# Kernel optimization log

Measured on AMD Instinct MI355X. Metric: run time of the kernel, lower is better.

Reference implementation:

```python
import math
import jax, jax.numpy as jnp
import numpy as np


def _skew(X, pad_value):
    # shift every row i one step right relative to row i-1: [B,M,L] -> [B,M,M+L]
    B, M, L = X.shape
    X = jnp.pad(X, ((0, 0), (0, 0), (0, M + 1)), constant_values=pad_value)
    X = X.reshape(B, -1)[:, :-M]
    return X.reshape(B, M, M + L)


def _unskew(X):
    # reverse of _skew: [B,M,M+L] -> [B,M,L]
    B, M, ML = X.shape
    L = ML - M
    X = X.reshape(B, -1)
    X = jnp.pad(X, ((0, 0), (0, M)))
    X = X.reshape(B, M, M + L + 1)
    return X[:, :, :L]


def setup_inputs() -> dict:
    key0 = jax.random.key(0)
    k1, k2, k3, k4 = jax.random.split(key0, 4)
    BH, M, D = 64, 1024, 64          # batch*heads, block len, head dim
    L = 1024                          # attn_span
    return {
        "query": jax.random.normal(k1, (BH, M, D), dtype=jnp.float32),
        "key": jax.random.normal(k2, (BH, M + L, D), dtype=jnp.float32),
        "value": jax.random.normal(k3, (BH, M + L, D), dtype=jnp.float32),
        "key_pe": jax.random.normal(k4, (1, D, L), dtype=jnp.float32),
    }


def reference(query, key, value, key_pe):
    hidden_size = query.shape[-1]
    # content scores: [BH, M, M+L] -> banded [BH, M, L]
    attn_cont = _unskew(jnp.matmul(query, jnp.swapaxes(key, -1, -2)))
    # relative position scores: [BH, M, L] (key_pe broadcasts over batch)
    attn_pos = jnp.matmul(query, key_pe)
    attn = (attn_cont + attn_pos) / math.sqrt(hidden_size)
    attn = jax.nn.softmax(attn, axis=-1)
    # dropout p=0.0 -> identity
    attn_skew = _skew(attn, 0.0)          # [BH, M, M+L]
    out = jnp.matmul(attn_skew, value)    # [BH, M, D]
    return out
```

## Files before the change

kernel.cpp:

```cpp
#include <hip/hip_runtime.h>
#include <hip/hip_bf16.h>


typedef __attribute__((ext_vector_type(8))) short bf16x8;
typedef __attribute__((ext_vector_type(4))) short bf16x4;
typedef __attribute__((ext_vector_type(4))) float f32x4;

#define BHN   64
#define MQ    1024
#define DH    64
#define LS    1024
#define NKEY  2048
#define NTILE 17

#define SZ_PE  ((size_t)LS * DH * 2)
#define OFF_K  SZ_PE
#define SZ_K   ((size_t)BHN * NKEY * DH * 2)
#define OFF_V  (OFF_K + SZ_K)
#define SZ_V   ((size_t)BHN * DH * NKEY * 2)
#define WS_NEED (OFF_V + SZ_V)

#define SCL_LOG2E 0.18033688011112042f

__device__ __forceinline__ short f2bf(float f) {
  unsigned u = __float_as_uint(f);
  u += 0x7FFFu + ((u >> 16) & 1u);
  return (short)(u >> 16);
}
__device__ __forceinline__ void async_copy16(const void* g, void* l) {
  __builtin_amdgcn_global_load_lds((const __attribute__((address_space(1))) void*)g,
                                   (__attribute__((address_space(3))) void*)l, 16, 0, 0);
}

__global__ void prep_pe_kernel(const float* __restrict__ pe, short* __restrict__ peT) {
  const int idx = blockIdx.x * 256 + threadIdx.x;
  const int rel = idx >> 6, d = idx & 63;
  peT[rel * 64 + (((d >> 3) ^ (rel & 7)) * 8) + (d & 7)] = f2bf(pe[d * LS + rel]);
}

__global__ void prep_k_kernel(const float* __restrict__ K, short* __restrict__ Kb) {
  const size_t i = ((size_t)blockIdx.x * 256 + threadIdx.x) * 4;
  const int row = (int)(i >> 6);
  const int col = (int)(i & 63);
  float4 f = *(const float4*)(K + i);
  bf16x4 b = {f2bf(f.x), f2bf(f.y), f2bf(f.z), f2bf(f.w)};
  *(bf16x4*)(Kb + (size_t)row * 64 + (((col >> 3) ^ (row & 7)) * 8) + (col & 7)) = b;
}

__global__ __launch_bounds__(256) void prep_v_kernel(const float* __restrict__ V,
                                                     short* __restrict__ Vb) {
  __shared__ short st[64 * 68];
  const int bh = blockIdx.y, jt = blockIdx.x;
  const int r = threadIdx.x >> 2, cb = (threadIdx.x & 3) * 16;
  const float* src = V + ((size_t)bh * NKEY + jt * 64 + r) * DH + cb;
#pragma unroll
  for (int c = 0; c < 16; c += 4) {
    float4 f = *(const float4*)(src + c);
    bf16x4 b = {f2bf(f.x), f2bf(f.y), f2bf(f.z), f2bf(f.w)};
    *(bf16x4*)&st[r * 68 + cb + c] = b;
  }
  __syncthreads();
  const int d = threadIdx.x >> 2, kb = (threadIdx.x & 3) * 16;
  __attribute__((aligned(16))) short tmp[16];
#pragma unroll
  for (int j = 0; j < 16; ++j) tmp[j] = st[(kb + j) * 68 + d];
  short* dst = Vb + ((size_t)bh * DH + d) * NKEY + jt * 64 + kb;
  *(bf16x8*)dst = *(bf16x8*)&tmp[0];
  *(bf16x8*)(dst + 8) = *(bf16x8*)&tmp[8];
}

template <bool PRECONV>
__global__ __launch_bounds__(256, 4)
void seq_attn_kernel(const float* __restrict__ Qf, const float* __restrict__ Kf,
                     const float* __restrict__ Vf, const short* __restrict__ peT,
                     const short* __restrict__ Kb, const short* __restrict__ Vb,
                     float* __restrict__ Out) {
  __shared__ short sK[64 * 64];
  __shared__ short sPE[2 * 64 * 64];
  __shared__ short sV[64 * 64];
  __shared__ short sPA[64 * 64];

  const int tid  = threadIdx.x;
  const int w    = tid >> 6;
  const int lane = tid & 63;
  const int li   = lane & 15;
  const int quad = lane >> 4;
  const int linear = blockIdx.y * 16 + blockIdx.x;
  const int slot   = linear >> 3;
  const int bh     = (linear & 7) * 8 + (slot >> 4);
  const int i0     = (slot & 15) * 64;
  const int rbase  = w * 16 + quad * 4;

  bf16x8 aq[2];
  {
    const float* qp = Qf + (size_t)((bh * MQ + i0 + w * 16 + li) * DH) + quad * 8;
#pragma unroll
    for (int ks = 0; ks < 2; ++ks) {
      const float4 f0 = *(const float4*)(qp + ks * 32);
      const float4 f1 = *(const float4*)(qp + ks * 32 + 4);
      bf16x8 a;
      a[0] = f2bf(f0.x); a[1] = f2bf(f0.y); a[2] = f2bf(f0.z); a[3] = f2bf(f0.w);
      a[4] = f2bf(f1.x); a[5] = f2bf(f1.y); a[6] = f2bf(f1.z); a[7] = f2bf(f1.w);
      aq[ks] = a;
    }
  }

  float l_i[4] = {0.f, 0.f, 0.f, 0.f};
  f32x4 acco[4];
#pragma unroll
  for (int nt = 0; nt < 4; ++nt) acco[nt] = (f32x4){0.f, 0.f, 0.f, 0.f};

  f32x4 curPw[4];
  f32x4 prevw3;
  prevw3 = (f32x4){0.f, 0.f, 0.f, 0.f};

  for (int t = 0; t < NTILE; ++t) {
    const int j0 = i0 + t * 64;
    __syncthreads();

    if constexpr (PRECONV) {
      {
        const char* gb = (const char*)(Kb + ((size_t)bh * NKEY + j0) * 64);
#pragma unroll
        for (int it = 0; it < 2; ++it) {
          const int c0 = w * 128 + it * 64;
          async_copy16(gb + (size_t)(c0 + lane) * 16, (char*)sK + (size_t)c0 * 16);
        }
      }
      if (t < NTILE - 1) {
        const char* gb = (const char*)(peT + (size_t)t * 64 * 64);
        char* db = (char*)sPE + (size_t)(t & 1) * 8192;
#pragma unroll
        for (int it = 0; it < 2; ++it) {
          const int c0 = w * 128 + it * 64;
          async_copy16(gb + (size_t)(c0 + lane) * 16, db + (size_t)c0 * 16);
        }
      }
      {
#pragma unroll
        for (int it = 0; it < 2; ++it) {
          const int s = w * 128 + it * 64 + lane;
          const int d = s >> 3;
          const int g = (s & 7) ^ (d & 7);
          const short* gp = Vb + ((size_t)bh * DH + d) * NKEY + j0 + g * 8;
          async_copy16(gp, (char*)sV + (size_t)(w * 128 + it * 64) * 16);
        }
      }
    } else {
      {
        const int srow = tid >> 2, l0 = tid & 3, sdb = l0 * 16;
        const float* src = Kf + (size_t)(bh * NKEY + j0 + srow) * DH + sdb;
        const float4 a0 = *(const float4*)(src + 0);
        const float4 a1 = *(const float4*)(src + 4);
        const float4 a2 = *(const float4*)(src + 8);
        const float4 a3 = *(const float4*)(src + 12);
        bf16x8 b0, b1;
        b0[0]=f2bf(a0.x); b0[1]=f2bf(a0.y); b0[2]=f2bf(a0.z); b0[3]=f2bf(a0.w);
        b0[4]=f2bf(a1.x); b0[5]=f2bf(a1.y); b0[6]=f2bf(a1.z); b0[7]=f2bf(a1.w);
        b1[0]=f2bf(a2.x); b1[1]=f2bf(a2.y); b1[2]=f2bf(a2.z); b1[3]=f2bf(a2.w);
        b1[4]=f2bf(a3.x); b1[5]=f2bf(a3.y); b1[6]=f2bf(a3.z); b1[7]=f2bf(a3.w);
        const int s7 = srow & 7;
        *(bf16x8*)&sK[srow * 64 + (((2 * l0)     ^ s7) * 8)] = b0;
        *(bf16x8*)&sK[srow * 64 + (((2 * l0 + 1) ^ s7) * 8)] = b1;
      }
      {
        const int vdb = (tid & 15) * 4, vkb = (tid >> 4) * 4;
        const float* src = Vf + (size_t)(bh * NKEY + j0 + vkb) * DH + vdb;
        const float4 r0 = *(const float4*)(src);
        const float4 r1 = *(const float4*)(src + DH);
        const float4 r2 = *(const float4*)(src + 2 * DH);
        const float4 r3 = *(const float4*)(src + 3 * DH);
        bf16x4 cc[4];
        cc[0] = (bf16x4){ f2bf(r0.x), f2bf(r1.x), f2bf(r2.x), f2bf(r3.x) };
        cc[1] = (bf16x4){ f2bf(r0.y), f2bf(r1.y), f2bf(r2.y), f2bf(r3.y) };
        cc[2] = (bf16x4){ f2bf(r0.z), f2bf(r1.z), f2bf(r2.z), f2bf(r3.z) };
        cc[3] = (bf16x4){ f2bf(r0.w), f2bf(r1.w), f2bf(r2.w), f2bf(r3.w) };
        const int g = vkb >> 3, h = (vkb >> 2) & 1;
#pragma unroll
        for (int jj = 0; jj < 4; ++jj) {
          const int d = vdb + jj;
          *(bf16x4*)&sV[d * 64 + ((g ^ (d & 7)) * 8) + h * 4] = cc[jj];
        }
      }
      if (t < NTILE - 1) {
        const short* src = peT + (size_t)t * 64 * 64;
        short* db = sPE + (size_t)(t & 1) * 4096;
        *(bf16x8*)&db[tid * 16]     = *(const bf16x8*)(src + tid * 16);
        *(bf16x8*)&db[tid * 16 + 8] = *(const bf16x8*)(src + tid * 16 + 8);
      }
    }
    __syncthreads();

#pragma unroll
    for (int m = 0; m < 4; ++m) {
      const int colIdx = 4 * t - w + m;
      const int base = ((colIdx >> 2) & 1) * 4096 + ((colIdx & 3) * 16 + li) * 64;
      f32x4 c = (f32x4){0.f, 0.f, 0.f, 0.f};
#pragma unroll
      for (int ks = 0; ks < 2; ++ks) {
        const int gs = (((ks * 4 + quad) ^ (li & 7)) * 8);
        const bf16x8 b = *(bf16x8*)&sPE[base + gs];
        c = __builtin_amdgcn_mfma_f32_16x16x32_bf16(aq[ks], b, c, 0, 0, 0);
      }
      curPw[m] = c;
    }

    f32x4 cs[4];
#pragma unroll
    for (int nt = 0; nt < 4; ++nt) {
      f32x4 c = (f32x4){0.f, 0.f, 0.f, 0.f};
#pragma unroll
      for (int ks = 0; ks < 2; ++ks) {
        const int gs = (((ks * 4 + quad) ^ (li & 7)) * 8);
        const bf16x8 b = *(bf16x8*)&sK[(nt * 16 + li) * 64 + gs];
        c = __builtin_amdgcn_mfma_f32_16x16x32_bf16(aq[ks], b, c, 0, 0, 0);
      }
      cs[nt] = c;
    }

#pragma unroll
    for (int r = 0; r < 4; ++r) {
      const int e       = li - quad * 4 - r;
      const bool ge     = (e >= 0);
      const int srcLane = quad * 16 + (e & 15);
      const float shm = __shfl(prevw3[r],    srcLane);
      const float sh0 = __shfl(curPw[0][r], srcLane);
      const float sh1 = __shfl(curPw[1][r], srcLane);
      const float sh2 = __shfl(curPw[2][r], srcLane);
      const float sh3 = __shfl(curPw[3][r], srcLane);
      const float pos0 = ge ? sh0 : shm;
      const float pos1 = ge ? sh1 : sh0;
      const float pos2 = ge ? sh2 : sh1;
      const float pos3 = ge ? sh3 : sh2;
      float p0 = __builtin_exp2f((cs[0][r] + pos0) * SCL_LOG2E);
      float p1 = __builtin_exp2f((cs[1][r] + pos1) * SCL_LOG2E);
      float p2 = __builtin_exp2f((cs[2][r] + pos2) * SCL_LOG2E);
      float p3 = __builtin_exp2f((cs[3][r] + pos3) * SCL_LOG2E);
      if (t == 0) {
        p0 = (0 > w || (0 == w && ge)) ? p0 : 0.f;
        p1 = (1 > w || (1 == w && ge)) ? p1 : 0.f;
        p2 = (2 > w || (2 == w && ge)) ? p2 : 0.f;
        p3 = (3 > w || (3 == w && ge)) ? p3 : 0.f;
      } else if (t == NTILE - 1) {
        p0 = (0 < w || (0 == w && !ge)) ? p0 : 0.f;
        p1 = (1 < w || (1 == w && !ge)) ? p1 : 0.f;
        p2 = (2 < w || (2 == w && !ge)) ? p2 : 0.f;
        p3 = (3 < w || (3 == w && !ge)) ? p3 : 0.f;
      }
      l_i[r] += (p0 + p1) + (p2 + p3);
      const int rowA = rbase + r;
      const int sw = (rowA >> 1) & 7;
      sPA[rowA * 64 + (((0 + (li >> 3)) ^ sw) * 8) + (li & 7)] = f2bf(p0);
      sPA[rowA * 64 + (((2 + (li >> 3)) ^ sw) * 8) + (li & 7)] = f2bf(p1);
      sPA[rowA * 64 + (((4 + (li >> 3)) ^ sw) * 8) + (li & 7)] = f2bf(p2);
      sPA[rowA * 64 + (((6 + (li >> 3)) ^ sw) * 8) + (li & 7)] = f2bf(p3);
    }
    prevw3 = curPw[3];

#pragma unroll
    for (int ks = 0; ks < 2; ++ks) {
      const int rowA = w * 16 + li;
      const bf16x8 ap =
          *(bf16x8*)&sPA[rowA * 64 + (((ks * 4 + quad) ^ ((rowA >> 1) & 7)) * 8)];
#pragma unroll
      for (int nt = 0; nt < 4; ++nt) {
        const int d  = nt * 16 + li;
        const int gs = (((ks * 4 + quad) ^ (d & 7)) * 8);
        const bf16x8 bv = *(bf16x8*)&sV[d * 64 + gs];
        acco[nt] = __builtin_amdgcn_mfma_f32_16x16x32_bf16(ap, bv, acco[nt], 0, 0, 0);
      }
    }
  }

#pragma unroll
  for (int r = 0; r < 4; ++r) {
    float l = l_i[r];
    l += __shfl_xor(l, 1);
    l += __shfl_xor(l, 2);
    l += __shfl_xor(l, 4);
    l += __shfl_xor(l, 8);
    const float inv = 1.0f / l;
#pragma unroll
    for (int nt = 0; nt < 4; ++nt) {
      Out[(size_t)(bh * MQ + i0 + rbase + r) * DH + nt * 16 + li] = acco[nt][r] * inv;
    }
  }
}

extern "C" void kernel_launch(void* const* d_in, const int* in_sizes, int n_in,
                              void* d_out, int out_size, void* d_ws, size_t ws_size,
                              hipStream_t stream) {
  const float* q  = (const float*)d_in[0];
  const float* k  = (const float*)d_in[1];
  const float* v  = (const float*)d_in[2];
  const float* pe = (const float*)d_in[3];
  float* out = (float*)d_out;
  short* peT = (short*)d_ws;
  short* Kb  = (short*)((char*)d_ws + OFF_K);
  short* Vb  = (short*)((char*)d_ws + OFF_V);
  const bool preconv = ws_size >= WS_NEED;

  prep_pe_kernel<<<256, 256, 0, stream>>>(pe, peT);
  dim3 grid(MQ / 64, BHN);
  if (preconv) {
    prep_k_kernel<<<8192, 256, 0, stream>>>(k, Kb);
    prep_v_kernel<<<dim3(32, 64), 256, 0, stream>>>(v, Vb);
    seq_attn_kernel<true><<<grid, 256, 0, stream>>>(q, k, v, peT, Kb, Vb, out);
  } else {
    seq_attn_kernel<false><<<grid, 256, 0, stream>>>(q, k, v, peT, Kb, Vb, out);
  }
}
```

Measured before the change: 182.5 us.

## Fuse prep kernels, permute P/V key order for vectorized LDS stores, bf16-pack shuffles

Merges the three preprocessing kernels (PE transpose, K convert, V transpose) into one launch that dispatches on block index, and gives the K conversion 16 elements per thread. The key ordering inside each 64-wide tile is permuted consistently in the V layout and in the P tile, so each lane writes its four probabilities with one 8-byte LDS store instead of four scalar stores. The four position-score shuffles are packed into two by sending pairs of bf16 values, which cuts cross-lane traffic but rounds those position scores to bf16 before they are added.

```diff
diff --git a/kernel.cpp b/kernel.cpp
--- a/kernel.cpp
+++ b/kernel.cpp
@@ -27,46 +27,72 @@
   u += 0x7FFFu + ((u >> 16) & 1u);
   return (short)(u >> 16);
 }
+__device__ __forceinline__ float bf2f(short s) {
+  return __uint_as_float(((unsigned)(unsigned short)s) << 16);
+}
+__device__ __forceinline__ unsigned packbf(float a, float b) {
+  return (unsigned)(unsigned short)f2bf(a) | ((unsigned)(unsigned short)f2bf(b) << 16);
+}
 __device__ __forceinline__ void async_copy16(const void* g, void* l) {
   __builtin_amdgcn_global_load_lds((const __attribute__((address_space(1))) void*)g,
                                    (__attribute__((address_space(3))) void*)l, 16, 0, 0);
 }
 
-__global__ void prep_pe_kernel(const float* __restrict__ pe, short* __restrict__ peT) {
-  const int idx = blockIdx.x * 256 + threadIdx.x;
-  const int rel = idx >> 6, d = idx & 63;
-  peT[rel * 64 + (((d >> 3) ^ (rel & 7)) * 8) + (d & 7)] = f2bf(pe[d * LS + rel]);
-}
-
-__global__ void prep_k_kernel(const float* __restrict__ K, short* __restrict__ Kb) {
-  const size_t i = ((size_t)blockIdx.x * 256 + threadIdx.x) * 4;
-  const int row = (int)(i >> 6);
-  const int col = (int)(i & 63);
-  float4 f = *(const float4*)(K + i);
-  bf16x4 b = {f2bf(f.x), f2bf(f.y), f2bf(f.z), f2bf(f.w)};
-  *(bf16x4*)(Kb + (size_t)row * 64 + (((col >> 3) ^ (row & 7)) * 8) + (col & 7)) = b;
-}
-
-__global__ __launch_bounds__(256) void prep_v_kernel(const float* __restrict__ V,
-                                                     short* __restrict__ Vb) {
+__global__ __launch_bounds__(256)
+void prep_fused(const float* __restrict__ pe, const float* __restrict__ K,
+                const float* __restrict__ V, short* __restrict__ peT,
+                short* __restrict__ Kb, short* __restrict__ Vb) {
   __shared__ short st[64 * 68];
-  const int bh = blockIdx.y, jt = blockIdx.x;
-  const int r = threadIdx.x >> 2, cb = (threadIdx.x & 3) * 16;
-  const float* src = V + ((size_t)bh * NKEY + jt * 64 + r) * DH + cb;
-#pragma unroll
-  for (int c = 0; c < 16; c += 4) {
-    float4 f = *(const float4*)(src + c);
-    bf16x4 b = {f2bf(f.x), f2bf(f.y), f2bf(f.z), f2bf(f.w)};
-    *(bf16x4*)&st[r * 68 + cb + c] = b;
-  }
-  __syncthreads();
-  const int d = threadIdx.x >> 2, kb = (threadIdx.x & 3) * 16;
-  __attribute__((aligned(16))) short tmp[16];
-#pragma unroll
-  for (int j = 0; j < 16; ++j) tmp[j] = st[(kb + j) * 68 + d];
-  short* dst = Vb + ((size_t)bh * DH + d) * NKEY + jt * 64 + kb;
-  *(bf16x8*)dst = *(bf16x8*)&tmp[0];
-  *(bf16x8*)(dst + 8) = *(bf16x8*)&tmp[8];
+  const int bx = blockIdx.x;
+  if (bx < 256) {
+    const int idx = bx * 256 + threadIdx.x;
+    const int rel = idx >> 6, d = idx & 63;
+    peT[rel * 64 + (((d >> 3) ^ (rel & 7)) * 8) + (d & 7)] = f2bf(pe[d * LS + rel]);
+  } else if (bx < 2304) {
+    const size_t i = ((size_t)(bx - 256) * 256 + threadIdx.x) * 16;
+    const int row = (int)(i >> 6);
+    const int c16 = (int)(i & 63);
+    const float4 f0 = *(const float4*)(K + i);
+    const float4 f1 = *(const float4*)(K + i + 4);
+    const float4 f2 = *(const float4*)(K + i + 8);
+    const float4 f3 = *(const float4*)(K + i + 12);
+    bf16x8 b0, b1;
+    b0[0]=f2bf(f0.x); b0[1]=f2bf(f0.y); b0[2]=f2bf(f0.z); b0[3]=f2bf(f0.w);
+    b0[4]=f2bf(f1.x); b0[5]=f2bf(f1.y); b0[6]=f2bf(f1.z); b0[7]=f2bf(f1.w);
+    b1[0]=f2bf(f2.x); b1[1]=f2bf(f2.y); b1[2]=f2bf(f2.z); b1[3]=f2bf(f2.w);
+    b1[4]=f2bf(f3.x); b1[5]=f2bf(f3.y); b1[6]=f2bf(f3.z); b1[7]=f2bf(f3.w);
+    const int s7 = row & 7;
+    short* dst = Kb + (size_t)row * 64;
+    *(bf16x8*)&dst[(((c16 >> 3))     ^ s7) * 8] = b0;
+    *(bf16x8*)&dst[(((c16 >> 3) + 1) ^ s7) * 8] = b1;
+  } else {
+    const int b  = bx - 2304;
+    const int bh = b >> 5, jt = b & 31;
+    {
+      const int r = threadIdx.x >> 2, cb = (threadIdx.x & 3) * 16;
+      const float* src = V + ((size_t)bh * NKEY + jt * 64 + r) * DH + cb;
+#pragma unroll
+      for (int c = 0; c < 16; c += 4) {
+        float4 f = *(const float4*)(src + c);
+        bf16x4 v = {f2bf(f.x), f2bf(f.y), f2bf(f.z), f2bf(f.w)};
+        *(bf16x4*)&st[r * 68 + cb + c] = v;
+      }
+    }
+    __syncthreads();
+    {
+      const int d = threadIdx.x >> 2, kapb = (threadIdx.x & 3) * 16;
+      __attribute__((aligned(16))) short tmp[16];
+#pragma unroll
+      for (int j = 0; j < 16; ++j) {
+        const int kap = kapb + j;
+        const int k   = (kap & 3) * 16 + (kap >> 2);
+        tmp[j] = st[k * 68 + d];
+      }
+      short* dst = Vb + ((size_t)bh * DH + d) * NKEY + jt * 64 + kapb;
+      *(bf16x8*)dst       = *(bf16x8*)&tmp[0];
+      *(bf16x8*)(dst + 8) = *(bf16x8*)&tmp[8];
+    }
+  }
 }
 
 template <bool PRECONV>
@@ -166,20 +192,17 @@
       {
         const int vdb = (tid & 15) * 4, vkb = (tid >> 4) * 4;
         const float* src = Vf + (size_t)(bh * NKEY + j0 + vkb) * DH + vdb;
-        const float4 r0 = *(const float4*)(src);
-        const float4 r1 = *(const float4*)(src + DH);
-        const float4 r2 = *(const float4*)(src + 2 * DH);
-        const float4 r3 = *(const float4*)(src + 3 * DH);
-        bf16x4 cc[4];
-        cc[0] = (bf16x4){ f2bf(r0.x), f2bf(r1.x), f2bf(r2.x), f2bf(r3.x) };
-        cc[1] = (bf16x4){ f2bf(r0.y), f2bf(r1.y), f2bf(r2.y), f2bf(r3.y) };
-        cc[2] = (bf16x4){ f2bf(r0.z), f2bf(r1.z), f2bf(r2.z), f2bf(r3.z) };
-        cc[3] = (bf16x4){ f2bf(r0.w), f2bf(r1.w), f2bf(r2.w), f2bf(r3.w) };
-        const int g = vkb >> 3, h = (vkb >> 2) & 1;
-#pragma unroll
-        for (int jj = 0; jj < 4; ++jj) {
-          const int d = vdb + jj;
-          *(bf16x4*)&sV[d * 64 + ((g ^ (d & 7)) * 8) + h * 4] = cc[jj];
+#pragma unroll
+        for (int m = 0; m < 4; ++m) {
+          const float4 rr = *(const float4*)(src + m * DH);
+          const int k   = vkb + m;
+          const int kap = (k & 15) * 4 + (k >> 4);
+#pragma unroll
+          for (int jj = 0; jj < 4; ++jj) {
+            const int d = vdb + jj;
+            const float fv = (jj == 0) ? rr.x : (jj == 1) ? rr.y : (jj == 2) ? rr.z : rr.w;
+            sV[d * 64 + (((kap >> 3) ^ (d & 7)) * 8) + (kap & 7)] = f2bf(fv);
+          }
         }
       }
       if (t < NTILE - 1) {
@@ -223,11 +246,15 @@
       const int e       = li - quad * 4 - r;
       const bool ge     = (e >= 0);
       const int srcLane = quad * 16 + (e & 15);
-      const float shm = __shfl(prevw3[r],    srcLane);
-      const float sh0 = __shfl(curPw[0][r], srcLane);
-      const float sh1 = __shfl(curPw[1][r], srcLane);
-      const float sh2 = __shfl(curPw[2][r], srcLane);
-      const float sh3 = __shfl(curPw[3][r], srcLane);
+      const float shm = __shfl(prevw3[r], srcLane);
+      const unsigned pk01 = packbf(curPw[0][r], curPw[1][r]);
+      const unsigned pk23 = packbf(curPw[2][r], curPw[3][r]);
+      const unsigned s01 = (unsigned)__shfl((int)pk01, srcLane);
+      const unsigned s23 = (unsigned)__shfl((int)pk23, srcLane);
+      const float sh0 = bf2f((short)(s01 & 0xffffu));
+      const float sh1 = bf2f((short)(s01 >> 16));
+      const float sh2 = bf2f((short)(s23 & 0xffffu));
+      const float sh3 = bf2f((short)(s23 >> 16));
       const float pos0 = ge ? sh0 : shm;
       const float pos1 = ge ? sh1 : sh0;
       const float pos2 = ge ? sh2 : sh1;
@@ -249,11 +276,8 @@
       }
       l_i[r] += (p0 + p1) + (p2 + p3);
       const int rowA = rbase + r;
-      const int sw = (rowA >> 1) & 7;
-      sPA[rowA * 64 + (((0 + (li >> 3)) ^ sw) * 8) + (li & 7)] = f2bf(p0);
-      sPA[rowA * 64 + (((2 + (li >> 3)) ^ sw) * 8) + (li & 7)] = f2bf(p1);
-      sPA[rowA * 64 + (((4 + (li >> 3)) ^ sw) * 8) + (li & 7)] = f2bf(p2);
-      sPA[rowA * 64 + (((6 + (li >> 3)) ^ sw) * 8) + (li & 7)] = f2bf(p3);
+      const bf16x4 pk = {f2bf(p0), f2bf(p1), f2bf(p2), f2bf(p3)};
+      *(bf16x4*)&sPA[rowA * 64 + (((li >> 1) ^ (rowA & 7)) * 8) + (li & 1) * 4] = pk;
     }
     prevw3 = curPw[3];
 
@@ -261,7 +285,7 @@
     for (int ks = 0; ks < 2; ++ks) {
       const int rowA = w * 16 + li;
       const bf16x8 ap =
-          *(bf16x8*)&sPA[rowA * 64 + (((ks * 4 + quad) ^ ((rowA >> 1) & 7)) * 8)];
+          *(bf16x8*)&sPA[rowA * 64 + (((ks * 4 + quad) ^ (rowA & 7)) * 8)];
 #pragma unroll
       for (int nt = 0; nt < 4; ++nt) {
         const int d  = nt * 16 + li;
@@ -300,13 +324,12 @@
   short* Vb  = (short*)((char*)d_ws + OFF_V);
   const bool preconv = ws_size >= WS_NEED;
 
-  prep_pe_kernel<<<256, 256, 0, stream>>>(pe, peT);
   dim3 grid(MQ / 64, BHN);
   if (preconv) {
-    prep_k_kernel<<<8192, 256, 0, stream>>>(k, Kb);
-    prep_v_kernel<<<dim3(32, 64), 256, 0, stream>>>(v, Vb);
+    prep_fused<<<4352, 256, 0, stream>>>(pe, k, v, peT, Kb, Vb);
     seq_attn_kernel<true><<<grid, 256, 0, stream>>>(q, k, v, peT, Kb, Vb, out);
   } else {
+    prep_fused<<<256, 256, 0, stream>>>(pe, k, v, peT, Kb, Vb);
     seq_attn_kernel<false><<<grid, 256, 0, stream>>>(q, k, v, peT, Kb, Vb, out);
   }
 }
```

New measurement: 178.0 us. -2.5%, faster.
